# Kernel tuning notes

Measured on AMD Instinct MI355X. Metric: run time of the kernel, lower is better.

Reference implementation:

```python
import jax, jax.numpy as jnp
import numpy as np

NUM_CLASSES = 1000
N, D = 65536, 512

def setup_inputs() -> dict:
    key = jax.random.key(0)
    k1, k2, k3 = jax.random.split(key, 3)
    x = jax.random.normal(k1, (N, D), dtype=jnp.float32)
    labels = jax.random.randint(k2, (N,), 0, NUM_CLASSES, dtype=jnp.int64)
    centers = jax.random.normal(k3, (NUM_CLASSES, D), dtype=jnp.float32)
    return {"x": x, "labels": labels, "centers": centers}

def reference(x, labels, centers):
    # diff of each sample to its own class center: [N, D]
    diff = x - centers[labels]
    # per-sample squared distance: [N]
    sq = jnp.sum(diff * diff, axis=-1)
    # segment-sum squared distances into classes, then Frobenius norm per class
    per_class_sq = jax.ops.segment_sum(sq, labels, num_segments=NUM_CLASSES)
    distance = jnp.sum(jnp.sqrt(per_class_sq))
    return distance / NUM_CLASSES
```

## Files before the change

kernel.cpp:

```cpp
#include <hip/hip_runtime.h>
#include <math.h>

#define NROWS 65536
#define DDIM 512
#define NUM_CLASSES 1000
#define NSHARD 8

__global__ __launch_bounds__(256) void CenterLoss_zero_ws(float* __restrict__ ws) {
    const int n = NSHARD * 1024;
    for (int i = threadIdx.x + blockIdx.x * 256; i < n; i += 256 * 8)
        ws[i] = 0.0f;
}

__device__ inline float sqdiff4(float4 a, float4 b) {
    float dx = a.x - b.x, dy = a.y - b.y, dz = a.z - b.z, dw = a.w - b.w;
    return fmaf(dx, dx, fmaf(dy, dy, fmaf(dz, dz, dw * dw)));
}

__global__ __launch_bounds__(256) void CenterLoss_accum(
    const float* __restrict__ x,
    const int* __restrict__ labels,
    const float* __restrict__ centers,
    float* __restrict__ ws)
{
    const int wave = threadIdx.x >> 6;
    const int lane = threadIdx.x & 63;
    const int row  = (blockIdx.x << 2) + wave;
    const int lbl  = labels[row];

    const float4* __restrict__ xr =
        reinterpret_cast<const float4*>(x + (size_t)row * DDIM);
    const float4* __restrict__ cr =
        reinterpret_cast<const float4*>(centers + (size_t)lbl * DDIM);

    const float4 xv0 = xr[lane];
    const float4 xv1 = xr[lane + 64];
    const float4 cv0 = cr[lane];
    const float4 cv1 = cr[lane + 64];

    float acc = sqdiff4(xv0, cv0) + sqdiff4(xv1, cv1);

#pragma unroll
    for (int off = 32; off > 0; off >>= 1)
        acc += __shfl_xor(acc, off, 64);

    if (lane == 0)
        atomicAdd(&ws[((blockIdx.x & (NSHARD - 1)) << 10) + lbl], acc);
}

__global__ __launch_bounds__(256) void CenterLoss_finalize(
    const float* __restrict__ ws, float* __restrict__ out)
{
    const int t = threadIdx.x;
    const int lane = t & 63;

    float s = 0.0f;
    if (t < NUM_CLASSES / 4) {
        float4 v = reinterpret_cast<const float4*>(ws)[t];
#pragma unroll
        for (int sh = 1; sh < NSHARD; ++sh) {
            float4 u = reinterpret_cast<const float4*>(ws + (sh << 10))[t];
            v.x += u.x; v.y += u.y; v.z += u.z; v.w += u.w;
        }
        s = sqrtf(v.x) + sqrtf(v.y) + sqrtf(v.z) + sqrtf(v.w);
    }
#pragma unroll
    for (int off = 32; off > 0; off >>= 1)
        s += __shfl_xor(s, off, 64);

    __shared__ float partial[4];
    if (lane == 0) partial[t >> 6] = s;
    __syncthreads();
    if (t == 0)
        out[0] = (partial[0] + partial[1] + partial[2] + partial[3])
                 / (float)NUM_CLASSES;
}

extern "C" void kernel_launch(void* const* d_in, const int* in_sizes, int n_in,
                              void* d_out, int out_size, void* d_ws, size_t ws_size,
                              hipStream_t stream) {
    const float* x       = (const float*)d_in[0];
    const int*   labels  = (const int*)d_in[1];
    const float* centers = (const float*)d_in[2];
    float* out = (float*)d_out;
    float* ws  = (float*)d_ws;

    CenterLoss_zero_ws<<<8, 256, 0, stream>>>(ws);
    CenterLoss_accum<<<NROWS / 4, 256, 0, stream>>>(x, labels, centers, ws);
    CenterLoss_finalize<<<1, 256, 0, stream>>>(ws, out);
}
```

Baseline: 36.87 us.

## Replace global atomic sharded accumulation with per-row store plus shared-memory binning

The main pass now writes each row's squared distance to workspace instead of issuing a global atomicAdd. A new 16-block kernel bins those values per class with shared-memory atomics and writes per-block partials, which finalize sums. This removes global atomic contention and the zero-init kernel, but adds an extra pass over 64K floats and labels in a low-parallelism kernel. If the workspace is too small, the code falls back to the old path.

```diff
diff --git a/kernel.cpp b/kernel.cpp
--- a/kernel.cpp
+++ b/kernel.cpp
@@ -4,20 +4,19 @@
 #define NROWS 65536
 #define DDIM 512
 #define NUM_CLASSES 1000
-#define NSHARD 8
 
-__global__ __launch_bounds__(256) void CenterLoss_zero_ws(float* __restrict__ ws) {
-    const int n = NSHARD * 1024;
-    for (int i = threadIdx.x + blockIdx.x * 256; i < n; i += 256 * 8)
-        ws[i] = 0.0f;
-}
+#define SQ_OFF 0
+#define PART_OFF NROWS
+#define NBIN_BLOCKS 16
+#define ROWS_PER_BIN_BLOCK (NROWS / NBIN_BLOCKS)
+#define WS_NEED ((size_t)(NROWS + NBIN_BLOCKS * NUM_CLASSES) * 4)
 
 __device__ inline float sqdiff4(float4 a, float4 b) {
     float dx = a.x - b.x, dy = a.y - b.y, dz = a.z - b.z, dw = a.w - b.w;
     return fmaf(dx, dx, fmaf(dy, dy, fmaf(dz, dz, dw * dw)));
 }
 
-__global__ __launch_bounds__(256) void CenterLoss_accum(
+__global__ __launch_bounds__(256) void CenterLoss_sq(
     const float* __restrict__ x,
     const int* __restrict__ labels,
     const float* __restrict__ centers,
@@ -45,7 +44,30 @@
         acc += __shfl_xor(acc, off, 64);
 
     if (lane == 0)
-        atomicAdd(&ws[((blockIdx.x & (NSHARD - 1)) << 10) + lbl], acc);
+        ws[SQ_OFF + row] = acc;
+}
+
+__global__ __launch_bounds__(1024) void CenterLoss_bin(
+    const int* __restrict__ labels,
+    float* __restrict__ ws)
+{
+    __shared__ float bins[NUM_CLASSES];
+    const int t = threadIdx.x;
+    if (t < NUM_CLASSES) bins[t] = 0.0f;
+    __syncthreads();
+
+    const int base = blockIdx.x * ROWS_PER_BIN_BLOCK;
+#pragma unroll
+    for (int i = 0; i < ROWS_PER_BIN_BLOCK / 1024; ++i) {
+        const int r = base + i * 1024 + t;
+        const float v = ws[SQ_OFF + r];
+        const int   l = labels[r];
+        atomicAdd(&bins[l], v);
+    }
+
+    __syncthreads();
+    if (t < NUM_CLASSES)
+        ws[PART_OFF + blockIdx.x * NUM_CLASSES + t] = bins[t];
 }
 
 __global__ __launch_bounds__(256) void CenterLoss_finalize(
@@ -56,10 +78,11 @@
 
     float s = 0.0f;
     if (t < NUM_CLASSES / 4) {
-        float4 v = reinterpret_cast<const float4*>(ws)[t];
+        float4 v = reinterpret_cast<const float4*>(ws + PART_OFF)[t];
 #pragma unroll
-        for (int sh = 1; sh < NSHARD; ++sh) {
-            float4 u = reinterpret_cast<const float4*>(ws + (sh << 10))[t];
+        for (int b = 1; b < NBIN_BLOCKS; ++b) {
+            float4 u = reinterpret_cast<const float4*>(
+                           ws + PART_OFF + (size_t)b * NUM_CLASSES)[t];
             v.x += u.x; v.y += u.y; v.z += u.z; v.w += u.w;
         }
         s = sqrtf(v.x) + sqrtf(v.y) + sqrtf(v.z) + sqrtf(v.w);
@@ -76,6 +99,51 @@
                  / (float)NUM_CLASSES;
 }
 
+#define NSHARD 8
+__global__ __launch_bounds__(256) void CL_zero8(float* __restrict__ ws) {
+    const int n = NSHARD * 1024;
+    for (int i = threadIdx.x + blockIdx.x * 256; i < n; i += 256 * 8) ws[i] = 0.0f;
+}
+__global__ __launch_bounds__(256) void CL_accum8(
+    const float* __restrict__ x, const int* __restrict__ labels,
+    const float* __restrict__ centers, float* __restrict__ ws)
+{
+    const int wave = threadIdx.x >> 6, lane = threadIdx.x & 63;
+    const int row = (blockIdx.x << 2) + wave;
+    const int lbl = labels[row];
+    const float4* xr = (const float4*)(x + (size_t)row * DDIM);
+    const float4* cr = (const float4*)(centers + (size_t)lbl * DDIM);
+    const float4 xv0 = xr[lane], xv1 = xr[lane + 64];
+    const float4 cv0 = cr[lane], cv1 = cr[lane + 64];
+    float acc = sqdiff4(xv0, cv0) + sqdiff4(xv1, cv1);
+#pragma unroll
+    for (int off = 32; off > 0; off >>= 1) acc += __shfl_xor(acc, off, 64);
+    if (lane == 0)
+        atomicAdd(&ws[((blockIdx.x & (NSHARD - 1)) << 10) + lbl], acc);
+}
+__global__ __launch_bounds__(256) void CL_final8(
+    const float* __restrict__ ws, float* __restrict__ out)
+{
+    const int t = threadIdx.x, lane = t & 63;
+    float s = 0.0f;
+    if (t < NUM_CLASSES / 4) {
+        float4 v = reinterpret_cast<const float4*>(ws)[t];
+#pragma unroll
+        for (int sh = 1; sh < NSHARD; ++sh) {
+            float4 u = reinterpret_cast<const float4*>(ws + (sh << 10))[t];
+            v.x += u.x; v.y += u.y; v.z += u.z; v.w += u.w;
+        }
+        s = sqrtf(v.x) + sqrtf(v.y) + sqrtf(v.z) + sqrtf(v.w);
+    }
+#pragma unroll
+    for (int off = 32; off > 0; off >>= 1) s += __shfl_xor(s, off, 64);
+    __shared__ float partial[4];
+    if (lane == 0) partial[t >> 6] = s;
+    __syncthreads();
+    if (t == 0)
+        out[0] = (partial[0] + partial[1] + partial[2] + partial[3]) / (float)NUM_CLASSES;
+}
+
 extern "C" void kernel_launch(void* const* d_in, const int* in_sizes, int n_in,
                               void* d_out, int out_size, void* d_ws, size_t ws_size,
                               hipStream_t stream) {
@@ -85,7 +153,13 @@
     float* out = (float*)d_out;
     float* ws  = (float*)d_ws;
 
-    CenterLoss_zero_ws<<<8, 256, 0, stream>>>(ws);
-    CenterLoss_accum<<<NROWS / 4, 256, 0, stream>>>(x, labels, centers, ws);
-    CenterLoss_finalize<<<1, 256, 0, stream>>>(ws, out);
+    if (ws_size >= WS_NEED) {
+        CenterLoss_sq<<<NROWS / 4, 256, 0, stream>>>(x, labels, centers, ws);
+        CenterLoss_bin<<<NBIN_BLOCKS, 1024, 0, stream>>>(labels, ws);
+        CenterLoss_finalize<<<1, 256, 0, stream>>>(ws, out);
+    } else {
+        CL_zero8<<<8, 256, 0, stream>>>(ws);
+        CL_accum8<<<NROWS / 4, 256, 0, stream>>>(x, labels, centers, ws);
+        CL_final8<<<1, 256, 0, stream>>>(ws, out);
+    }
 }
```

Result: slower. 38.47 us (+4.3%).
